# Performance work log

Measured on AMD Instinct MI355X. Metric: run time of the kernel, lower is better.

The kernel has to match this reference:

```python
import jax, jax.numpy as jnp
import numpy as np

EPS = 1e-8
C_RGLRU = 8.0  # Griffin constant

def rmsnorm(x, w):
    rms = jnp.sqrt(jnp.mean(x * x, axis=-1, keepdims=True) + EPS)
    return w * (x / rms)

def causal_depthwise_conv(x, conv_w, conv_b):
    # x: [B,S,H], conv_w: [K,H] depthwise causal conv, left-padded
    K = conv_w.shape[0]
    S = x.shape[1]
    xp = jnp.pad(x, ((0, 0), (K - 1, 0), (0, 0)))
    y = sum(conv_w[k] * xp[:, k:k + S, :] for k in range(K))
    return y + conv_b

def rg_lru(x, ga_W, ga_b, gx_W, gx_b, a_param):
    # x: [B,S,H]. Griffin RG-LRU: h_t = a_t h_{t-1} + sqrt(1-a_t^2) (i_t * x_t)
    r = jax.nn.sigmoid(x @ ga_W + ga_b)          # recurrence gate
    i = jax.nn.sigmoid(x @ gx_W + gx_b)          # input gate
    log_a = -C_RGLRU * jax.nn.softplus(a_param) * r
    a = jnp.exp(log_a)
    mult = jnp.sqrt(-jnp.expm1(2.0 * log_a))     # sqrt(1 - a^2), stable
    b = mult * (i * x)
    def combine(c1, c2):
        a1, b1 = c1
        a2, b2 = c2
        return a1 * a2, a2 * b1 + b2
    _, h = jax.lax.associative_scan(combine, (a, b), axis=1)
    return h

def setup_inputs() -> dict:
    D, H, F, K, B, S = 2048, 2048, 6144, 4, 2, 2048
    key = jax.random.key(0)
    ks = jax.random.split(key, 16)
    def lin(k, fan_in, shape):
        return jax.random.normal(k, shape, jnp.float32) * (fan_in ** -0.5)
    return {
        "x": jax.random.normal(ks[0], (B, S, D), jnp.float32),
        "norm1_w": jnp.ones((D,), jnp.float32),
        "left_W": lin(ks[1], D, (D, H)), "left_b": jnp.zeros((H,), jnp.float32),
        "right_W": lin(ks[2], D, (D, H)), "right_b": jnp.zeros((H,), jnp.float32),
        "conv_w": lin(ks[3], K, (K, H)), "conv_b": jnp.zeros((H,), jnp.float32),
        "ga_W": lin(ks[4], H, (H, H)), "ga_b": jnp.zeros((H,), jnp.float32),
        "gx_W": lin(ks[5], H, (H, H)), "gx_b": jnp.zeros((H,), jnp.float32),
        "a_param": jax.random.uniform(ks[6], (H,), jnp.float32, 0.5, 3.0),
        "out_W": lin(ks[7], H, (H, D)), "out_b": jnp.zeros((D,), jnp.float32),
        "norm2_w": jnp.ones((D,), jnp.float32),
        "up1_W": lin(ks[8], D, (D, F)), "up1_b": jnp.zeros((F,), jnp.float32),
        "up2_W": lin(ks[9], D, (D, F)), "up2_b": jnp.zeros((F,), jnp.float32),
        "down_W": lin(ks[10], F, (F, D)), "down_b": jnp.zeros((D,), jnp.float32),
    }

def reference(x, norm1_w, left_W, left_b, right_W, right_b, conv_w, conv_b,
              ga_W, ga_b, gx_W, gx_b, a_param, out_W, out_b,
              norm2_w, up1_W, up1_b, up2_W, up2_b, down_W, down_b):
    gelu = lambda t: jax.nn.gelu(t, approximate=False)
    # recurrent sub-block (pre-norm residual)
    xn = rmsnorm(x, norm1_w)
    left = gelu(xn @ left_W + left_b)
    right = rg_lru(causal_depthwise_conv(xn @ right_W + right_b, conv_w, conv_b),
                   ga_W, ga_b, gx_W, gx_b, a_param)
    x1 = (left * right) @ out_W + out_b + x
    # gated MLP sub-block (pre-norm residual)
    x1n = rmsnorm(x1, norm2_w)
    mlp = (gelu(x1n @ up1_W + up1_b) * (x1n @ up2_W + up2_b)) @ down_W + down_b
    return mlp + x1
```

## Files before the change

kernel.cpp:

```cpp
#include <hip/hip_runtime.h>
#include <cstdint>
#include <cstdio>

typedef __bf16 bf16x8 __attribute__((ext_vector_type(8)));
typedef float  f32x4  __attribute__((ext_vector_type(4)));
typedef const __attribute__((address_space(1))) void* gas_ptr;
typedef __attribute__((address_space(3))) void* las_ptr;

__device__ __forceinline__ uint16_t f32_to_bf16_rne(float f){
  uint32_t u = __builtin_bit_cast(uint32_t, f);
  u += 0x7FFFu + ((u >> 16) & 1u);
  return (uint16_t)(u >> 16);
}
__device__ __forceinline__ float bf16_to_f32(uint16_t h){
  uint32_t u = (uint32_t)h << 16;
  return __builtin_bit_cast(float, u);
}
__device__ __forceinline__ float gelu_exact(float x){
  return 0.5f * x * (1.f + erff(x * 0.7071067811865475f));
}

template<int EPI>
__device__ __forceinline__ void epi_store(float v, size_t idx, int row, int col,
    int N, int SPLIT, const float* auxF, const uint16_t* auxB,
    float* Cf, uint16_t* Cb0, uint16_t* Cb1, bool second)
{
  if constexpr (EPI == 1) {
    if (!second) Cb0[(size_t)row * SPLIT + col] = f32_to_bf16_rne(gelu_exact(v));
    else         Cb1[(size_t)row * (N - SPLIT) + (col - SPLIT)] = f32_to_bf16_rne(v);
  }
  if constexpr (EPI == 2) Cb0[idx] = f32_to_bf16_rne(v);
  if constexpr (EPI == 4) Cb0[idx] = f32_to_bf16_rne(v + auxF[idx]);
  if constexpr (EPI == 5) Cf[idx] = v + bf16_to_f32(auxB[idx]);
}

template<int EPI>
__global__ __launch_bounds__(512)
void gemm8p(const uint16_t* __restrict__ A, const uint16_t* __restrict__ Bt,
            const float* __restrict__ bias0, const float* __restrict__ bias1,
            const float* __restrict__ auxF, const uint16_t* __restrict__ auxB,
            float* __restrict__ Cf, uint16_t* __restrict__ Cb0, uint16_t* __restrict__ Cb1,
            int M, int N, int K, int SPLIT)
{
  __shared__ alignas(16) char smem[131072];
  const int tid = threadIdx.x, lane = tid & 63, wid = tid >> 6;
  const int wm = wid >> 2, wn = wid & 3;
  const int la = lane & 15, lq = lane >> 4;
  const int n0 = blockIdx.x * 256, m0 = blockIdx.y * 256;

  const int rt = tid >> 3;
  const int gs = (tid & 7) ^ (rt & 7);
  const uint16_t* srcA = A  + (size_t)(m0 + rt) * K + gs * 8;
  const uint16_t* srcB = Bt + (size_t)(n0 + rt) * K + gs * 8;

  const int rowAb = (wm * 128 + la) * 128;
  const int rowBb = (wn * 64 + la) * 128;
  const int ck0 = ((lq)     ^ (la & 7)) * 16;
  const int ck1 = ((4 + lq) ^ (la & 7)) * 16;

  f32x4 acc[8][4];
  const f32x4 fz = {0.f, 0.f, 0.f, 0.f};
#pragma unroll
  for (int m = 0; m < 8; ++m)
#pragma unroll
    for (int n = 0; n < 4; ++n) acc[m][n] = fz;

  bf16x8 aF[4][2], bF0[2][2], bF1[2][2];
  const int NT = K >> 6;

#define STAGE_A8(KT, BUF) do { _Pragma("unroll")                              \
    for (int l = 0; l < 4; ++l)                                               \
      __builtin_amdgcn_global_load_lds(                                       \
          (gas_ptr)(srcA + (size_t)(KT) * 64 + (size_t)l * 64 * K),           \
          (las_ptr)(smem + (BUF) * 32768 + (l * 512 + tid) * 16), 16, 0, 0);  \
  } while (0)
#define STAGE_B8(KT, BUF) do { _Pragma("unroll")                              \
    for (int l = 0; l < 4; ++l)                                               \
      __builtin_amdgcn_global_load_lds(                                       \
          (gas_ptr)(srcB + (size_t)(KT) * 64 + (size_t)l * 64 * K),           \
          (las_ptr)(smem + 65536 + (BUF) * 32768 + (l * 512 + tid) * 16),     \
          16, 0, 0);                                                          \
  } while (0)
#define RD_B8(DST, NH, BUF) do { _Pragma("unroll")                            \
    for (int nq = 0; nq < 2; ++nq) {                                          \
      int ro_ = 65536 + (BUF) * 32768 + rowBb + ((NH) * 2 + nq) * 2048;       \
      DST[nq][0] = *(const bf16x8*)(smem + ro_ + ck0);                        \
      DST[nq][1] = *(const bf16x8*)(smem + ro_ + ck1);                        \
    }                                                                         \
  } while (0)
#define RD_A8(MHS, BUF) do { _Pragma("unroll")                                \
    for (int mq = 0; mq < 4; ++mq) {                                          \
      int ro_ = (BUF) * 32768 + rowAb + ((MHS) * 4 + mq) * 2048;              \
      aF[mq][0] = *(const bf16x8*)(smem + ro_ + ck0);                         \
      aF[mq][1] = *(const bf16x8*)(smem + ro_ + ck1);                         \
    }                                                                         \
  } while (0)
#define MM8(MHS, NH, BF) do { _Pragma("unroll")                               \
    for (int mq = 0; mq < 4; ++mq)                                            \
      _Pragma("unroll")                                                       \
      for (int nq = 0; nq < 2; ++nq) {                                        \
        acc[(MHS)*4+mq][(NH)*2+nq] = __builtin_amdgcn_mfma_f32_16x16x32_bf16( \
            aF[mq][0], BF[nq][0], acc[(MHS)*4+mq][(NH)*2+nq], 0, 0, 0);       \
        acc[(MHS)*4+mq][(NH)*2+nq] = __builtin_amdgcn_mfma_f32_16x16x32_bf16( \
            aF[mq][1], BF[nq][1], acc[(MHS)*4+mq][(NH)*2+nq], 0, 0, 0);       \
      }                                                                       \
  } while (0)
#define BARR() __builtin_amdgcn_s_barrier()

  STAGE_A8(0, 0); STAGE_B8(0, 0);
  STAGE_A8(1, 1); STAGE_B8(1, 1);
  asm volatile("s_waitcnt vmcnt(8)" ::: "memory");
  BARR();

  for (int t = 0; t < NT; ++t) {
    const int buf = t & 1;
    const bool pf = (t + 2 < NT);
    RD_B8(bF0, 0, buf); RD_A8(0, buf);
    BARR();
    __builtin_amdgcn_s_setprio(1); MM8(0, 0, bF0); __builtin_amdgcn_s_setprio(0);
    BARR();
    RD_B8(bF1, 1, buf);
    BARR();
    __builtin_amdgcn_s_setprio(1); MM8(0, 1, bF1); __builtin_amdgcn_s_setprio(0);
    BARR();
    RD_A8(1, buf);
    if (pf) STAGE_B8(t + 2, buf);
    BARR();
    __builtin_amdgcn_s_setprio(1); MM8(1, 0, bF0); __builtin_amdgcn_s_setprio(0);
    BARR();
    if (pf) STAGE_A8(t + 2, buf);
    BARR();
    __builtin_amdgcn_s_setprio(1); MM8(1, 1, bF1); __builtin_amdgcn_s_setprio(0);
    asm volatile("s_waitcnt vmcnt(8)" ::: "memory");
    BARR();
  }
#undef STAGE_A8
#undef STAGE_B8
#undef RD_B8
#undef RD_A8
#undef MM8
#undef BARR

#pragma unroll
  for (int n = 0; n < 4; ++n) {
    int col = n0 + wn * 64 + n * 16 + la;
    const bool second = (col >= SPLIT);
    float bv = second ? bias1[col - SPLIT] : bias0[col];
#pragma unroll
    for (int m = 0; m < 8; ++m) {
      int rbase = m0 + wm * 128 + m * 16 + lq * 4;
#pragma unroll
      for (int r = 0; r < 4; ++r) {
        int row = rbase + r;
        size_t idx = (size_t)row * N + col;
        epi_store<EPI>(acc[m][n][r] + bv, idx, row, col, N, SPLIT, auxF, auxB, Cf, Cb0, Cb1, second);
      }
    }
  }
}

template<int EPI, int BM>
__global__ __launch_bounds__(512)
void gemm2p(const uint16_t* __restrict__ A, const uint16_t* __restrict__ Bt,
            const float* __restrict__ bias0, const float* __restrict__ bias1,
            const float* __restrict__ auxF, const uint16_t* __restrict__ auxB,
            float* __restrict__ Cf, uint16_t* __restrict__ Cb0, uint16_t* __restrict__ Cb1,
            int M, int N, int K, int SPLIT)
{
  constexpr int BN = 256;
  constexpr int M_REP   = BM / 32;
  constexpr int LOADS_A = BM / 64;
  constexpr int LOADS_B = BN / 64;
  constexpr int ABYTES  = 2 * BM * 128;
  __shared__ alignas(16) char smem[2 * (BM + BN) * 128];

  const int tid  = threadIdx.x;
  const int lane = tid & 63;
  const int wid  = tid >> 6;
  const int wm = wid >> 2, wn = wid & 3;
  const int la = lane & 15, lq = lane >> 4;
  const int n0 = blockIdx.x * BN;
  const int m0 = blockIdx.y * BM;

  const int rt = tid >> 3;
  const int gs = (tid & 7) ^ (rt & 7);
  const uint16_t* srcA = A  + (size_t)(m0 + rt) * K + gs * 8;
  const uint16_t* srcB = Bt + (size_t)(n0 + rt) * K + gs * 8;

  const int rowAb = (wm * (BM / 2) + la) * 128;
  const int rowBb = (wn * 64 + la) * 128;
  const int ck0 = ((lq)     ^ (la & 7)) * 16;
  const int ck1 = ((4 + lq) ^ (la & 7)) * 16;

  f32x4 acc[M_REP][4];
  const f32x4 fz = {0.f, 0.f, 0.f, 0.f};
#pragma unroll
  for (int m = 0; m < M_REP; ++m)
#pragma unroll
    for (int n = 0; n < 4; ++n) acc[m][n] = fz;

  const int NT = K >> 6;

#define STAGE(KT, BUF) do {                                                   \
    const uint16_t* sa_ = srcA + (size_t)(KT) * 64;                           \
    const uint16_t* sb_ = srcB + (size_t)(KT) * 64;                           \
    _Pragma("unroll")                                                         \
    for (int l = 0; l < LOADS_A; ++l)                                         \
      __builtin_amdgcn_global_load_lds((gas_ptr)(sa_ + (size_t)l * 64 * K),   \
          (las_ptr)(smem + (BUF) * BM * 128 + (l * 512 + tid) * 16), 16, 0, 0);\
    _Pragma("unroll")                                                         \
    for (int l = 0; l < LOADS_B; ++l)                                         \
      __builtin_amdgcn_global_load_lds((gas_ptr)(sb_ + (size_t)l * 64 * K),   \
          (las_ptr)(smem + ABYTES + (BUF) * BN * 128 + (l * 512 + tid) * 16), \
          16, 0, 0);                                                          \
  } while (0)

  STAGE(0, 0);
  asm volatile("s_waitcnt vmcnt(0)" ::: "memory");
  __builtin_amdgcn_s_barrier();

  int cur = 0;
  for (int kt = 0; kt < NT; ++kt) {
    const bool pf = (kt + 1 < NT);
    if (pf) STAGE(kt + 1, cur ^ 1);

    const int offA = cur * BM * 128;
    const int offB = ABYTES + cur * BN * 128;

    bf16x8 bF[4][2];
#pragma unroll
    for (int n = 0; n < 4; ++n) {
      int ro = offB + rowBb + n * 2048;
      bF[n][0] = *(const bf16x8*)(smem + ro + ck0);
      bF[n][1] = *(const bf16x8*)(smem + ro + ck1);
    }
    __builtin_amdgcn_s_setprio(1);
#pragma unroll
    for (int m = 0; m < M_REP; ++m) {
      int ro = offA + rowAb + m * 2048;
      bf16x8 a0 = *(const bf16x8*)(smem + ro + ck0);
      bf16x8 a1 = *(const bf16x8*)(smem + ro + ck1);
#pragma unroll
      for (int n = 0; n < 4; ++n) {
        acc[m][n] = __builtin_amdgcn_mfma_f32_16x16x32_bf16(a0, bF[n][0], acc[m][n], 0, 0, 0);
        acc[m][n] = __builtin_amdgcn_mfma_f32_16x16x32_bf16(a1, bF[n][1], acc[m][n], 0, 0, 0);
      }
    }
    __builtin_amdgcn_s_setprio(0);

    if (pf) {
      asm volatile("s_waitcnt vmcnt(0)" ::: "memory");
      __builtin_amdgcn_s_barrier();
      cur ^= 1;
    }
  }
#undef STAGE

#pragma unroll
  for (int n = 0; n < 4; ++n) {
    int col = n0 + wn * 64 + n * 16 + la;
    const bool second = (col >= SPLIT);
    float bv = second ? bias1[col - SPLIT] : bias0[col];
#pragma unroll
    for (int m = 0; m < M_REP; ++m) {
      int rbase = m0 + wm * (BM / 2) + m * 16 + lq * 4;
#pragma unroll
      for (int r = 0; r < 4; ++r) {
        int row = rbase + r;
        size_t idx = (size_t)row * N + col;
        epi_store<EPI>(acc[m][n][r] + bv, idx, row, col, N, SPLIT, auxF, auxB, Cf, Cb0, Cb1, second);
      }
    }
  }
}

__global__ __launch_bounds__(256)
void cvt_transpose(const float* __restrict__ in, uint16_t* __restrict__ out, int R, int C)
{
  __shared__ float tile[64][65];
  const int r0 = blockIdx.y * 64, c0 = blockIdx.x * 64;
  const int t = threadIdx.x;
  const int lc = (t & 15) * 4;
  const int lr0 = t >> 4;
#pragma unroll
  for (int j = 0; j < 4; j++){
    int lr = lr0 + j*16;
    float4 v = *(const float4*)(in + (size_t)(r0 + lr) * C + c0 + lc);
    tile[lr][lc+0] = v.x; tile[lr][lc+1] = v.y; tile[lr][lc+2] = v.z; tile[lr][lc+3] = v.w;
  }
  __syncthreads();
  const int oc = t >> 2;
  const int rseg = (t & 3) * 16;
  alignas(16) uint16_t tmp[16];
#pragma unroll
  for (int j = 0; j < 16; j++) tmp[j] = f32_to_bf16_rne(tile[rseg + j][oc]);
  uint4* dst = (uint4*)(out + (size_t)(c0 + oc) * R + r0 + rseg);
  dst[0] = *(const uint4*)(&tmp[0]);
  dst[1] = *(const uint4*)(&tmp[8]);
}

__global__ __launch_bounds__(256)
void rmsnorm_kernel(const float* __restrict__ x, const float* __restrict__ w,
                    uint16_t* __restrict__ out, int D)
{
  const int row = blockIdx.x;
  const float* xr = x + (size_t)row * D;
  const int base = threadIdx.x * 8;
  float4 va = *(const float4*)(xr + base);
  float4 vb = *(const float4*)(xr + base + 4);
  float ss = va.x*va.x + va.y*va.y + va.z*va.z + va.w*va.w
           + vb.x*vb.x + vb.y*vb.y + vb.z*vb.z + vb.w*vb.w;
#pragma unroll
  for (int o = 32; o > 0; o >>= 1) ss += __shfl_xor(ss, o);
  __shared__ float red[4];
  if ((threadIdx.x & 63) == 0) red[threadIdx.x >> 6] = ss;
  __syncthreads();
  float tot = red[0] + red[1] + red[2] + red[3];
  float inv = rsqrtf(tot / (float)D + 1e-8f);
  float4 wa = *(const float4*)(w + base);
  float4 wb = *(const float4*)(w + base + 4);
  alignas(16) uint16_t tmp[8];
  tmp[0] = f32_to_bf16_rne(va.x * wa.x * inv);
  tmp[1] = f32_to_bf16_rne(va.y * wa.y * inv);
  tmp[2] = f32_to_bf16_rne(va.z * wa.z * inv);
  tmp[3] = f32_to_bf16_rne(va.w * wa.w * inv);
  tmp[4] = f32_to_bf16_rne(vb.x * wb.x * inv);
  tmp[5] = f32_to_bf16_rne(vb.y * wb.y * inv);
  tmp[6] = f32_to_bf16_rne(vb.z * wb.z * inv);
  tmp[7] = f32_to_bf16_rne(vb.w * wb.w * inv);
  *(uint4*)(out + (size_t)row * D + base) = *(const uint4*)tmp;
}

__global__ __launch_bounds__(256)
void rmsnorm_bf16_kernel(const uint16_t* __restrict__ x, const float* __restrict__ w,
                         uint16_t* __restrict__ out, int D)
{
  const int row = blockIdx.x;
  const uint16_t* xr = x + (size_t)row * D;
  const int base = threadIdx.x * 8;
  uint4 v = *(const uint4*)(xr + base);
  const uint16_t* vp = (const uint16_t*)&v;
  float xs[8];
  float ss = 0.f;
#pragma unroll
  for (int j = 0; j < 8; ++j){ xs[j] = bf16_to_f32(vp[j]); ss += xs[j]*xs[j]; }
#pragma unroll
  for (int o = 32; o > 0; o >>= 1) ss += __shfl_xor(ss, o);
  __shared__ float red[4];
  if ((threadIdx.x & 63) == 0) red[threadIdx.x >> 6] = ss;
  __syncthreads();
  float tot = red[0] + red[1] + red[2] + red[3];
  float inv = rsqrtf(tot / (float)D + 1e-8f);
  float4 wa = *(const float4*)(w + base);
  float4 wb = *(const float4*)(w + base + 4);
  float wv[8] = {wa.x, wa.y, wa.z, wa.w, wb.x, wb.y, wb.z, wb.w};
  alignas(16) uint16_t tmp[8];
#pragma unroll
  for (int j = 0; j < 8; ++j) tmp[j] = f32_to_bf16_rne(xs[j] * wv[j] * inv);
  *(uint4*)(out + (size_t)row * D + base) = *(const uint4*)tmp;
}

__global__ __launch_bounds__(256)
void mul_kernel(uint16_t* __restrict__ t1, const uint16_t* __restrict__ u2)
{
  size_t i = ((size_t)blockIdx.x * 256 + threadIdx.x) * 8;
  uint4 a = *(const uint4*)(t1 + i);
  uint4 b = *(const uint4*)(u2 + i);
  const uint16_t* ap = (const uint16_t*)&a;
  const uint16_t* bp = (const uint16_t*)&b;
  alignas(16) uint16_t o[8];
#pragma unroll
  for (int j = 0; j < 8; ++j)
    o[j] = f32_to_bf16_rne(bf16_to_f32(ap[j]) * bf16_to_f32(bp[j]));
  *(uint4*)(t1 + i) = *(const uint4*)o;
}

__global__ __launch_bounds__(256)
void conv_kernel(const uint16_t* __restrict__ xin, const float* __restrict__ cw,
                 const float* __restrict__ cb, uint16_t* __restrict__ yout,
                 int S, int H)
{
  const int h = blockIdx.x * 256 + threadIdx.x;
  const int b = blockIdx.z;
  const int t0 = blockIdx.y * 128;
  const float w0 = cw[h], w1 = cw[H + h], w2 = cw[2*H + h], w3 = cw[3*H + h];
  const float bias = cb[h];
  const size_t colbase = (size_t)b * S * H + h;
  float xm3 = (t0 >= 3) ? bf16_to_f32(xin[colbase + (size_t)(t0-3)*H]) : 0.f;
  float xm2 = (t0 >= 2) ? bf16_to_f32(xin[colbase + (size_t)(t0-2)*H]) : 0.f;
  float xm1 = (t0 >= 1) ? bf16_to_f32(xin[colbase + (size_t)(t0-1)*H]) : 0.f;
  for (int t = t0; t < t0 + 128; ++t){
    size_t idx = colbase + (size_t)t * H;
    float xt = bf16_to_f32(xin[idx]);
    float y = w0*xm3 + w1*xm2 + w2*xm1 + w3*xt + bias;
    yout[idx] = f32_to_bf16_rne(y);
    xm3 = xm2; xm2 = xm1; xm1 = xt;
  }
}

__device__ __forceinline__ void rglru_ab(float rp, float ip, float xc, float coef,
                                         float& a, float& bb)
{
  float r  = 1.f / (1.f + expf(-rp));
  float la = coef * r;
  a = expf(la);
  float mult = sqrtf(-expm1f(2.f * la));
  float ig = 1.f / (1.f + expf(-ip));
  bb = mult * ig * xc;
}

__global__ __launch_bounds__(256)
void scan_phase1(const uint16_t* __restrict__ gpre, const uint16_t* __restrict__ convb,
                 const float* __restrict__ ap,
                 float* __restrict__ SA, float* __restrict__ SB,
                 int S, int H, int T0, int NC)
{
  const int h = blockIdx.x * 256 + threadIdx.x;
  const int j = blockIdx.y, b = blockIdx.z;
  const float coef = -8.f * log1pf(expf(ap[h]));
  size_t rowb = (size_t)b * S + (size_t)j * T0;
  float A = 1.f, Bc = 0.f;
  for (int t = 0; t < T0; ++t){
    size_t row = rowb + t;
    float rp = bf16_to_f32(gpre[row * 2 * H + h]);
    float ip = bf16_to_f32(gpre[row * 2 * H + H + h]);
    float xc = bf16_to_f32(convb[row * H + h]);
    float a, bb; rglru_ab(rp, ip, xc, coef, a, bb);
    A *= a; Bc = a * Bc + bb;
  }
  size_t o = ((size_t)b * NC + j) * H + h;
  SA[o] = A; SB[o] = Bc;
}

__global__ __launch_bounds__(256)
void scan_phase2(const float* __restrict__ SA, const float* __restrict__ SB,
                 float* __restrict__ SH, int H, int NC)
{
  const int h = blockIdx.x * 256 + threadIdx.x;
  const int b = blockIdx.y;
  float hh = 0.f;
  for (int j = 0; j < NC; ++j){
    size_t o = ((size_t)b * NC + j) * H + h;
    SH[o] = hh;
    hh = SA[o] * hh + SB[o];
  }
}

__global__ __launch_bounds__(256)
void scan_phase3(const uint16_t* __restrict__ gpre, const uint16_t* __restrict__ convb,
                 const float* __restrict__ ap, const float* __restrict__ SH,
                 const uint16_t* __restrict__ left, uint16_t* __restrict__ lr,
                 int S, int H, int T0, int NC)
{
  const int h = blockIdx.x * 256 + threadIdx.x;
  const int j = blockIdx.y, b = blockIdx.z;
  const float coef = -8.f * log1pf(expf(ap[h]));
  float hh = SH[((size_t)b * NC + j) * H + h];
  size_t rowb = (size_t)b * S + (size_t)j * T0;
  for (int t = 0; t < T0; ++t){
    size_t row = rowb + t;
    float rp = bf16_to_f32(gpre[row * 2 * H + h]);
    float ip = bf16_to_f32(gpre[row * 2 * H + H + h]);
    float xc = bf16_to_f32(convb[row * H + h]);
    float a, bb; rglru_ab(rp, ip, xc, coef, a, bb);
    hh = a * hh + bb;
    lr[row * H + h] = f32_to_bf16_rne(bf16_to_f32(left[row * H + h]) * hh);
  }
}

extern "C" void kernel_launch(void* const* d_in, const int* in_sizes, int n_in,
                              void* d_out, int out_size, void* d_ws, size_t ws_size,
                              hipStream_t stream)
{
  const int B = 2, S = 2048, D = 2048, H = 2048, F = 6144;
  const int M = B * S;
  const int NC = 32, T0 = S / NC;

  const float* x       = (const float*)d_in[0];
  const float* norm1_w = (const float*)d_in[1];
  const float* left_W  = (const float*)d_in[2];
  const float* left_b  = (const float*)d_in[3];
  const float* right_W = (const float*)d_in[4];
  const float* right_b = (const float*)d_in[5];
  const float* conv_w  = (const float*)d_in[6];
  const float* conv_b  = (const float*)d_in[7];
  const float* ga_W    = (const float*)d_in[8];
  const float* ga_b    = (const float*)d_in[9];
  const float* gx_W    = (const float*)d_in[10];
  const float* gx_b    = (const float*)d_in[11];
  const float* a_param = (const float*)d_in[12];
  const float* out_W   = (const float*)d_in[13];
  const float* out_b   = (const float*)d_in[14];
  const float* norm2_w = (const float*)d_in[15];
  const float* up1_W   = (const float*)d_in[16];
  const float* up1_b   = (const float*)d_in[17];
  const float* up2_W   = (const float*)d_in[18];
  const float* up2_b   = (const float*)d_in[19];
  const float* down_W  = (const float*)d_in[20];
  const float* down_b  = (const float*)d_in[21];

  char* ws = (char*)d_ws;
  size_t off = 0;
  auto alloc = [&](size_t bytes) -> char* {
    char* p = ws + off; off += (bytes + 255) & ~(size_t)255; return p;
  };
  uint16_t* WT    = (uint16_t*)alloc((size_t)2 * F * D * 2);
  uint16_t* XN    = (uint16_t*)alloc((size_t)M * D * 2);
  uint16_t* LEFT  = (uint16_t*)alloc((size_t)M * H * 2);
  uint16_t* RPRE  = (uint16_t*)alloc((size_t)M * H * 2);
  uint16_t* CONVB = (uint16_t*)alloc((size_t)M * H * 2);
  uint16_t* GPRE  = (uint16_t*)alloc((size_t)M * 2 * H * 2);
  uint16_t* LR    = (uint16_t*)alloc((size_t)M * H * 2);
  uint16_t* X1B   = (uint16_t*)alloc((size_t)M * D * 2);
  uint16_t* X1N   = (uint16_t*)alloc((size_t)M * D * 2);
  float*    SA    = (float*)   alloc((size_t)B * NC * H * 4);
  float*    SB    = (float*)   alloc((size_t)B * NC * H * 4);
  float*    SHB   = (float*)   alloc((size_t)B * NC * H * 4);
  uint16_t* T1    = XN;
  uint16_t* U2    = CONVB;

  if (off > ws_size) {
    fprintf(stderr, "kernel_launch: ws too small, need %zu have %zu\n", off, ws_size);
    return;
  }

  float* OUT = (float*)d_out;
  dim3 blk(256);
  dim3 gblk(512);

  rmsnorm_kernel<<<M, blk, 0, stream>>>(x, norm1_w, XN, D);

  cvt_transpose<<<dim3(H/64, D/64), blk, 0, stream>>>(left_W, WT, D, H);
  cvt_transpose<<<dim3(H/64, D/64), blk, 0, stream>>>(right_W, WT + (size_t)H * D, D, H);
  gemm8p<1><<<dim3((2*H)/256, M/256), gblk, 0, stream>>>(
      XN, WT, left_b, right_b, nullptr, nullptr, nullptr, LEFT, RPRE, M, 2*H, D, H);

  conv_kernel<<<dim3(H/256, S/128, B), blk, 0, stream>>>(RPRE, conv_w, conv_b, CONVB, S, H);

  cvt_transpose<<<dim3(H/64, H/64), blk, 0, stream>>>(ga_W, WT, H, H);
  cvt_transpose<<<dim3(H/64, H/64), blk, 0, stream>>>(gx_W, WT + (size_t)H * H, H, H);
  gemm8p<2><<<dim3((2*H)/256, M/256), gblk, 0, stream>>>(
      CONVB, WT, ga_b, gx_b, nullptr, nullptr, nullptr, GPRE, nullptr, M, 2*H, H, H);

  scan_phase1<<<dim3(H/256, NC, B), blk, 0, stream>>>(GPRE, CONVB, a_param, SA, SB, S, H, T0, NC);
  scan_phase2<<<dim3(H/256, B), blk, 0, stream>>>(SA, SB, SHB, H, NC);
  scan_phase3<<<dim3(H/256, NC, B), blk, 0, stream>>>(GPRE, CONVB, a_param, SHB, LEFT, LR, S, H, T0, NC);

  cvt_transpose<<<dim3(D/64, H/64), blk, 0, stream>>>(out_W, WT, H, D);
  gemm2p<4, 128><<<dim3(D/256, M/128), gblk, 0, stream>>>(
      LR, WT, out_b, out_b, x, nullptr, nullptr, X1B, nullptr, M, D, H, D);

  rmsnorm_bf16_kernel<<<M, blk, 0, stream>>>(X1B, norm2_w, X1N, D);

  cvt_transpose<<<dim3(F/64, D/64), blk, 0, stream>>>(up1_W, WT, D, F);
  cvt_transpose<<<dim3(F/64, D/64), blk, 0, stream>>>(up2_W, WT + (size_t)F * D, D, F);
  gemm8p<1><<<dim3((2*F)/256, M/256), gblk, 0, stream>>>(
      X1N, WT, up1_b, up2_b, nullptr, nullptr, nullptr, T1, U2, M, 2*F, D, F);

  mul_kernel<<<dim3((unsigned)((size_t)M * F / 8 / 256)), blk, 0, stream>>>(T1, U2);

  cvt_transpose<<<dim3(D/64, F/64), blk, 0, stream>>>(down_W, WT, F, D);
  gemm2p<5, 128><<<dim3(D/256, M/128), gblk, 0, stream>>>(
      T1, WT, down_b, down_b, nullptr, X1B, OUT, nullptr, nullptr, M, D, F, D);
}
```

Before: 782.8 us.

## Fuse GeGLU multiply into up-projection GEMM via interleaved weight columns

Interleaves the transposed up1 and up2 weights in 16-column groups so each warp's accumulator tile holds matching columns from both projections. A new GEMM epilogue then computes gelu(up1)*up2 directly and writes a single bf16 gated tensor. This removes the separate elementwise multiply kernel and the write and re-read of two M×F intermediates. The cost is a heavier epilogue with erf per output pair and a special weight layout.

```diff
diff --git a/kernel.cpp b/kernel.cpp
--- a/kernel.cpp
+++ b/kernel.cpp
@@ -141,19 +141,39 @@
 #undef MM8
 #undef BARR
 
-#pragma unroll
-  for (int n = 0; n < 4; ++n) {
-    int col = n0 + wn * 64 + n * 16 + la;
-    const bool second = (col >= SPLIT);
-    float bv = second ? bias1[col - SPLIT] : bias0[col];
-#pragma unroll
-    for (int m = 0; m < 8; ++m) {
-      int rbase = m0 + wm * 128 + m * 16 + lq * 4;
-#pragma unroll
-      for (int r = 0; r < 4; ++r) {
-        int row = rbase + r;
-        size_t idx = (size_t)row * N + col;
-        epi_store<EPI>(acc[m][n][r] + bv, idx, row, col, N, SPLIT, auxF, auxB, Cf, Cb0, Cb1, second);
+  if constexpr (EPI == 6) {
+    const int GN = N >> 1;
+#pragma unroll
+    for (int np = 0; np < 2; ++np) {
+      int gcol = (n0 >> 1) + wn * 32 + np * 16 + la;
+      float b1 = bias0[gcol], b2 = bias1[gcol];
+#pragma unroll
+      for (int m = 0; m < 8; ++m) {
+        int rbase = m0 + wm * 128 + m * 16 + lq * 4;
+#pragma unroll
+        for (int r = 0; r < 4; ++r) {
+          int row = rbase + r;
+          float v1 = acc[m][2*np][r] + b1;
+          float v2 = acc[m][2*np+1][r] + b2;
+          Cb0[(size_t)row * GN + gcol] = f32_to_bf16_rne(gelu_exact(v1) * v2);
+        }
+      }
+    }
+  } else {
+#pragma unroll
+    for (int n = 0; n < 4; ++n) {
+      int col = n0 + wn * 64 + n * 16 + la;
+      const bool second = (col >= SPLIT);
+      float bv = second ? bias1[col - SPLIT] : bias0[col];
+#pragma unroll
+      for (int m = 0; m < 8; ++m) {
+        int rbase = m0 + wm * 128 + m * 16 + lq * 4;
+#pragma unroll
+        for (int r = 0; r < 4; ++r) {
+          int row = rbase + r;
+          size_t idx = (size_t)row * N + col;
+          epi_store<EPI>(acc[m][n][r] + bv, idx, row, col, N, SPLIT, auxF, auxB, Cf, Cb0, Cb1, second);
+        }
       }
     }
   }
@@ -295,6 +315,34 @@
 #pragma unroll
   for (int j = 0; j < 16; j++) tmp[j] = f32_to_bf16_rne(tile[rseg + j][oc]);
   uint4* dst = (uint4*)(out + (size_t)(c0 + oc) * R + r0 + rseg);
+  dst[0] = *(const uint4*)(&tmp[0]);
+  dst[1] = *(const uint4*)(&tmp[8]);
+}
+
+__global__ __launch_bounds__(256)
+void cvt_transpose_ileave(const float* __restrict__ in, uint16_t* __restrict__ out,
+                          int R, int C, int half)
+{
+  __shared__ float tile[64][65];
+  const int r0 = blockIdx.y * 64, c0 = blockIdx.x * 64;
+  const int t = threadIdx.x;
+  const int lc = (t & 15) * 4;
+  const int lr0 = t >> 4;
+#pragma unroll
+  for (int j = 0; j < 4; j++){
+    int lr = lr0 + j*16;
+    float4 v = *(const float4*)(in + (size_t)(r0 + lr) * C + c0 + lc);
+    tile[lr][lc+0] = v.x; tile[lr][lc+1] = v.y; tile[lr][lc+2] = v.z; tile[lr][lc+3] = v.w;
+  }
+  __syncthreads();
+  const int oc = t >> 2;
+  const int rseg = (t & 3) * 16;
+  const int c = c0 + oc;
+  const int wrow = ((c >> 4) << 5) + half * 16 + (c & 15);
+  alignas(16) uint16_t tmp[16];
+#pragma unroll
+  for (int j = 0; j < 16; j++) tmp[j] = f32_to_bf16_rne(tile[rseg + j][oc]);
+  uint4* dst = (uint4*)(out + (size_t)wrow * R + r0 + rseg);
   dst[0] = *(const uint4*)(&tmp[0]);
   dst[1] = *(const uint4*)(&tmp[8]);
 }
@@ -358,21 +406,6 @@
 #pragma unroll
   for (int j = 0; j < 8; ++j) tmp[j] = f32_to_bf16_rne(xs[j] * wv[j] * inv);
   *(uint4*)(out + (size_t)row * D + base) = *(const uint4*)tmp;
-}
-
-__global__ __launch_bounds__(256)
-void mul_kernel(uint16_t* __restrict__ t1, const uint16_t* __restrict__ u2)
-{
-  size_t i = ((size_t)blockIdx.x * 256 + threadIdx.x) * 8;
-  uint4 a = *(const uint4*)(t1 + i);
-  uint4 b = *(const uint4*)(u2 + i);
-  const uint16_t* ap = (const uint16_t*)&a;
-  const uint16_t* bp = (const uint16_t*)&b;
-  alignas(16) uint16_t o[8];
-#pragma unroll
-  for (int j = 0; j < 8; ++j)
-    o[j] = f32_to_bf16_rne(bf16_to_f32(ap[j]) * bf16_to_f32(bp[j]));
-  *(uint4*)(t1 + i) = *(const uint4*)o;
 }
 
 __global__ __launch_bounds__(256)
@@ -516,8 +549,7 @@
   float*    SA    = (float*)   alloc((size_t)B * NC * H * 4);
   float*    SB    = (float*)   alloc((size_t)B * NC * H * 4);
   float*    SHB   = (float*)   alloc((size_t)B * NC * H * 4);
-  uint16_t* T1    = XN;
-  uint16_t* U2    = CONVB;
+  uint16_t* G     = XN;
 
   if (off > ws_size) {
     fprintf(stderr, "kernel_launch: ws too small, need %zu have %zu\n", off, ws_size);
@@ -552,14 +584,12 @@
 
   rmsnorm_bf16_kernel<<<M, blk, 0, stream>>>(X1B, norm2_w, X1N, D);
 
-  cvt_transpose<<<dim3(F/64, D/64), blk, 0, stream>>>(up1_W, WT, D, F);
-  cvt_transpose<<<dim3(F/64, D/64), blk, 0, stream>>>(up2_W, WT + (size_t)F * D, D, F);
-  gemm8p<1><<<dim3((2*F)/256, M/256), gblk, 0, stream>>>(
-      X1N, WT, up1_b, up2_b, nullptr, nullptr, nullptr, T1, U2, M, 2*F, D, F);
-
-  mul_kernel<<<dim3((unsigned)((size_t)M * F / 8 / 256)), blk, 0, stream>>>(T1, U2);
+  cvt_transpose_ileave<<<dim3(F/64, D/64), blk, 0, stream>>>(up1_W, WT, D, F, 0);
+  cvt_transpose_ileave<<<dim3(F/64, D/64), blk, 0, stream>>>(up2_W, WT, D, F, 1);
+  gemm8p<6><<<dim3((2*F)/256, M/256), gblk, 0, stream>>>(
+      X1N, WT, up1_b, up2_b, nullptr, nullptr, nullptr, G, nullptr, M, 2*F, D, 2*F);
 
   cvt_transpose<<<dim3(D/64, F/64), blk, 0, stream>>>(down_W, WT, F, D);
   gemm2p<5, 128><<<dim3(D/256, M/128), gblk, 0, stream>>>(
-      T1, WT, down_b, down_b, nullptr, X1B, OUT, nullptr, nullptr, M, D, F, D);
-}
+      G, WT, down_b, down_b, nullptr, X1B, OUT, nullptr, nullptr, M, D, F, D);
+}
```

Measured after the change: 731.0 us. -6.6%, faster.
